# Performance work log

Measured on AMD Instinct MI355X. Metric: run time of the kernel, lower is better.

The kernel has to match this reference:

```python
import jax, jax.numpy as jnp
import numpy as np

I_SZ, H_SZ, M_SZ, D_SZ, T_LEN = 256, 512, 16384, 256, 128


def setup_inputs() -> dict:
    key = jax.random.key(0)
    ks = iter(jax.random.split(key, 48))

    def rn(shape, s=0.05):
        return jax.random.normal(next(ks), shape, dtype=jnp.float32) * s

    Hd, D = H_SZ, D_SZ
    inp = {
        "inputs": rn((T_LEN, 1, I_SZ), 1.0),
        "memory0": rn((M_SZ, D), 0.01),            # register_buffer: randn*0.01
        "read_w0": jnp.zeros((M_SZ,), jnp.float32),
        "write_w0": jnp.zeros((M_SZ,), jnp.float32),
        "W_ih": rn((4 * Hd, I_SZ + D)),             # LSTM input->gates (i,f,g,o)
        "W_hh": rn((4 * Hd, Hd)),
        "b_ih": jnp.zeros((4 * Hd,), jnp.float32),
        "b_hh": jnp.zeros((4 * Hd,), jnp.float32),
        "Wo": rn((I_SZ, Hd + D)),                   # output_layer
        "bo": jnp.zeros((I_SZ,), jnp.float32),
    }
    for p in ("r", "w"):  # read head / write head addressing params
        inp[p + "_Wk"] = rn((D, Hd)); inp[p + "_bk"] = jnp.zeros((D,), jnp.float32)
        inp[p + "_Wb"] = rn((1, Hd)); inp[p + "_bb"] = jnp.zeros((1,), jnp.float32)
        inp[p + "_Wg"] = rn((1, Hd)); inp[p + "_bg"] = jnp.zeros((1,), jnp.float32)
        inp[p + "_Ws"] = rn((3, Hd)); inp[p + "_bs"] = jnp.zeros((3,), jnp.float32)
        inp[p + "_Wp"] = rn((1, Hd)); inp[p + "_bp"] = jnp.zeros((1,), jnp.float32)
    inp["w_We"] = rn((D, Hd)); inp["w_be"] = jnp.zeros((D,), jnp.float32)  # erase
    inp["w_Wa"] = rn((D, Hd)); inp["w_ba"] = jnp.zeros((D,), jnp.float32)  # add
    return inp


def _attend(co, mem, prev_w, Wk, bk, Wb, bb, Wg, bg, Ws, bs, Wp, bp):
    # co: (1,H), mem: (M,D), prev_w: (M,) -> (M,)
    key = co @ Wk.T + bk                                   # (1,D)
    beta = jax.nn.softplus(co @ Wb.T + bb)                 # (1,1) key strength
    kn = key / jnp.maximum(jnp.linalg.norm(key, axis=-1, keepdims=True), 1e-12)
    mn = mem / jnp.maximum(jnp.linalg.norm(mem, axis=-1, keepdims=True), 1e-12)
    cw = jax.nn.softmax(beta * (kn @ mn.T), axis=-1)       # (1,M) content weights
    g = jax.nn.sigmoid(co @ Wg.T + bg)                     # interpolation gate
    gw = g * cw + (1.0 - g) * prev_w[None, :]
    s = jax.nn.softmax(co @ Ws.T + bs, axis=-1)            # (1,3) shift kernel
    shifted = (s[:, 0:1] * jnp.roll(gw, -1, axis=-1)
               + s[:, 1:2] * gw
               + s[:, 2:3] * jnp.roll(gw, 1, axis=-1))
    gamma = jax.nn.softplus(co @ Wp.T + bp) + 1.0          # sharpening >= 1
    w = shifted ** gamma
    return (w / (w.sum(-1, keepdims=True) + 1e-8))[0]


def reference(inputs, memory0, read_w0, write_w0, W_ih, W_hh, b_ih, b_hh, Wo, bo,
              r_Wk, r_bk, r_Wb, r_bb, r_Wg, r_bg, r_Ws, r_bs, r_Wp, r_bp,
              w_Wk, w_bk, w_Wb, w_bb, w_Wg, w_bg, w_Ws, w_bs, w_Wp, w_bp,
              w_We, w_be, w_Wa, w_ba):
    H = W_hh.shape[1]

    def step(carry, x_t):
        mem, rw, ww, h, c = carry
        read_vec = rw @ mem                                  # (D,) read old memory
        ci = jnp.concatenate([x_t[0], read_vec])[None, :]    # (1, I+D)
        gates = ci @ W_ih.T + b_ih + h @ W_hh.T + b_hh       # (1, 4H)
        i_, f_, g_, o_ = jnp.split(gates, 4, axis=-1)
        c_new = jax.nn.sigmoid(f_) * c + jax.nn.sigmoid(i_) * jnp.tanh(g_)
        h_new = jax.nn.sigmoid(o_) * jnp.tanh(c_new)
        co = h_new                                           # controller output (1,H)
        ww_new = _attend(co, mem, ww, w_Wk, w_bk, w_Wb, w_bb, w_Wg, w_bg, w_Ws, w_bs, w_Wp, w_bp)
        erase = jax.nn.sigmoid(co @ w_We.T + w_be)[0]        # (D,)
        add = (co @ w_Wa.T + w_ba)[0]                        # (D,)
        mem_new = mem * (1.0 - ww_new[:, None] * erase[None, :]) + ww_new[:, None] * add[None, :]
        rw_new = _attend(co, mem_new, rw, r_Wk, r_bk, r_Wb, r_bb, r_Wg, r_bg, r_Ws, r_bs, r_Wp, r_bp)
        out = jnp.concatenate([co[0], read_vec])[None, :] @ Wo.T + bo  # (1, I)
        return (mem_new, rw_new, ww_new, h_new, c_new), out

    init = (memory0, read_w0, write_w0,
            jnp.zeros((1, H), inputs.dtype), jnp.zeros((1, H), inputs.dtype))
    _, outs = jax.lax.scan(step, init, inputs)               # (T,1,I)
    return outs
```

## Files before the change

kernel.cpp:

```cpp
#include <hip/hip_runtime.h>
#include <math.h>


#define NBLK 128
#define NTHR 512
#define Msz  16384
#define Dsz  256
#define Hsz  512
#define Isz  256
#define Tlen 128
#define RPB  128
#define NG   16
#define PUBSTR 8

struct Params { const float* in[34]; float* out; float* ws; };

__device__ __forceinline__ float wred64(float v){
#pragma unroll
  for (int o = 32; o > 0; o >>= 1) v += __shfl_xor(v, o, 64);
  return v;
}
__device__ __forceinline__ float wred32(float v){
#pragma unroll
  for (int o = 16; o > 0; o >>= 1) v += __shfl_xor(v, o, 32);
  return v;
}
__device__ __forceinline__ float qsum4(float v){
  v += __uint_as_float(__builtin_amdgcn_mov_dpp(__float_as_uint(v), 0xB1, 0xF, 0xF, true));
  v += __uint_as_float(__builtin_amdgcn_mov_dpp(__float_as_uint(v), 0x4E, 0xF, 0xF, true));
  return v;
}
__device__ __forceinline__ float sigm(float x){ return 1.f / (1.f + __expf(-x)); }
__device__ __forceinline__ float softplusf(float x){ return (x > 20.f) ? x : log1pf(__expf(x)); }

__device__ __forceinline__ void gstore(float* p, float v){
  __hip_atomic_store(p, v, __ATOMIC_RELAXED, __HIP_MEMORY_SCOPE_AGENT);
}
__device__ __forceinline__ float gload(const float* p){
  return __hip_atomic_load(p, __ATOMIC_RELAXED, __HIP_MEMORY_SCOPE_AGENT);
}
__device__ __forceinline__ void gstore64(unsigned long long* p, unsigned long long v){
  __hip_atomic_store(p, v, __ATOMIC_RELAXED, __HIP_MEMORY_SCOPE_AGENT);
}
__device__ __forceinline__ unsigned long long gload64(const unsigned long long* p){
  return __hip_atomic_load(p, __ATOMIC_RELAXED, __HIP_MEMORY_SCOPE_AGENT);
}
__device__ __forceinline__ void lbar(){
  __builtin_amdgcn_s_waitcnt(0xC07F);
  __builtin_amdgcn_s_barrier();
}
__device__ __forceinline__ float pollw(const unsigned long long* p, unsigned want){
  unsigned long long k;
  do { k = gload64(p); } while ((int)((unsigned)(k >> 32) - want) < 0);
  return __uint_as_float((unsigned)k);
}

__global__ void __launch_bounds__(NTHR, 1)
ntm_kernel(Params P)
{
  const int b   = blockIdx.x;
  const int tid = threadIdx.x;
  const int wv  = tid >> 6;
  const int ln  = tid & 63;

  const float* inputs  = P.in[0];
  const float* mem0    = P.in[1];
  const float* read_w0 = P.in[2];
  const float* write_w0= P.in[3];
  const float* W_ih = P.in[4];
  const float* W_hh = P.in[5];
  const float* b_ih = P.in[6];
  const float* b_hh = P.in[7];
  const float* Wo   = P.in[8];
  const float* bo   = P.in[9];
  const float* r_Wk = P.in[10]; const float* r_bk = P.in[11];
  const float* r_Wb = P.in[12]; const float* r_bb = P.in[13];
  const float* r_Wg = P.in[14]; const float* r_bg = P.in[15];
  const float* r_Ws = P.in[16]; const float* r_bs = P.in[17];
  const float* r_Wp = P.in[18]; const float* r_bp = P.in[19];
  const float* w_Wk = P.in[20]; const float* w_bk = P.in[21];
  const float* w_Wb = P.in[22]; const float* w_bb = P.in[23];
  const float* w_Wg = P.in[24]; const float* w_bg = P.in[25];
  const float* w_Ws = P.in[26]; const float* w_bs = P.in[27];
  const float* w_Wp = P.in[28]; const float* w_bp = P.in[29];
  const float* w_We = P.in[30]; const float* w_be = P.in[31];
  const float* w_Wa = P.in[32]; const float* w_ba = P.in[33];
  float* out = P.out;

  float* ws = P.ws;
  float* PA = ws;
  float* PB = ws + 4096;
  unsigned long long* U    = (unsigned long long*)(ws + 8192);
  unsigned long long* hpub = U;
  unsigned long long* ppub = U + 1024;
  unsigned long long* pubD = U + 2320;
  unsigned long long* pubF = pubD + 1024;
  unsigned long long* pubH = pubF + 1024;
  unsigned long long* pubJ = pubH + 1024;
  unsigned long long* wEF = pubJ + 1024;
  unsigned long long* wPF = wEF + 128;
  unsigned long long* wEL = wPF + 128;
  unsigned long long* wPL = wEL + 128;
  unsigned long long* rEF = wPL + 128;
  unsigned long long* rPF = rEF + 128;
  unsigned long long* rEL = rPF + 128;
  unsigned long long* rPL = rEL + 128;
  float* Pbuf[2] = { PA, PB };

  __shared__ float s_mem[RPB * Dsz];
  __shared__ float s_co[Hsz];
  __shared__ float s_a[256], s_b[256], s_c[256];
  __shared__ float s_rv[256];
  __shared__ float s_norm[RPB];
  __shared__ float s_e[RPB];
  __shared__ float s_bw[RPB];
  __shared__ float s_rw[RPB];
  __shared__ float s_ww[RPB];
  __shared__ float s_A1[RPB], s_A2[RPB], s_B1[RPB], s_B0[RPB];
  __shared__ float s_dot[RPB];
  __shared__ float s_red[8];
  __shared__ float s_lg[16];
  __shared__ float s_scal[16];
  __shared__ float s_w2[2];
  __shared__ float s_cst[4];
  __shared__ float s_bd[4];
  __shared__ float s_pub;
  __shared__ float s_gval;

  auto pubWaitSum = [&](unsigned long long* pub, unsigned want)->float{
    if (wv == 0){
      const unsigned long long* p0 = &pub[(size_t)ln * PUBSTR];
      const unsigned long long* p1 = &pub[(size_t)(64 + ln) * PUBSTR];
      unsigned long long k0, k1;
      for (;;){
        k0 = gload64(p0); k1 = gload64(p1);
        bool ok = ((int)((unsigned)(k0 >> 32) - want) >= 0) &&
                  ((int)((unsigned)(k1 >> 32) - want) >= 0);
        if (__all(ok)) break;
      }
      float acc = __uint_as_float((unsigned)k0) + __uint_as_float((unsigned)k1);
      acc = wred64(acc);
      if (ln == 0) s_gval = acc;
    }
    lbar();
    return s_gval;
  };

  auto bred512 = [&](float v)->float{
    v = wred64(v);
    lbar();
    if (ln == 0) s_red[wv] = v;
    lbar();
    return s_red[0] + s_red[1] + s_red[2] + s_red[3]
         + s_red[4] + s_red[5] + s_red[6] + s_red[7];
  };

  auto shiftSharpen = [&](int si, float* s_prevw, float S,
                          unsigned long long* pub, unsigned tag){
    float g     = sigm(s_scal[si + 1]);
    float gamma = softplusf(s_scal[si + 2]) + 1.f;
    float a0 = s_scal[si + 3], a1 = s_scal[si + 4], a2 = s_scal[si + 5];
    float mx = fmaxf(a0, fmaxf(a1, a2));
    float e0 = __expf(a0 - mx), e1 = __expf(a1 - mx), e2 = __expf(a2 - mx);
    float idn = 1.f / (e0 + e1 + e2);
    float s0 = e0 * idn, s1 = e1 * idn, s2 = e2 * idn;
    float invS = 1.f / S;
    float w = 0.f;
    if (tid < RPB){
      float gc = g * invS, gp = 1.f - g;
      float em = s_e[tid],  pm = s_prevw[tid];
      float e1n = (tid < RPB-1) ? s_e[tid+1]     : s_bd[0];
      float p1n = (tid < RPB-1) ? s_prevw[tid+1] : s_bd[1];
      float e2n = (tid > 0)     ? s_e[tid-1]     : s_bd[2];
      float p2n = (tid > 0)     ? s_prevw[tid-1] : s_bd[3];
      float gwm = gc * em  + gp * pm;
      float gw1 = gc * e1n + gp * p1n;
      float gw2 = gc * e2n + gp * p2n;
      float sh = s0 * gw1 + s1 * gwm + s2 * gw2;
      w = powf(sh, gamma);
      s_bw[tid] = w;
    }
    float tot = wred64(w);
    if (ln == 0 && wv < 2) s_w2[wv] = tot;
    lbar();
    if (tid == 0){
      float T2 = s_w2[0] + s_w2[1];
      s_pub = T2;
      if (pub) gstore64(&pub[(size_t)b * PUBSTR],
                        ((unsigned long long)tag << 32) | (unsigned long long)__float_as_uint(T2));
    }
  };

  auto gemvXH = [&]()->float{
    int dd = tid >> 5, l = tid & 31;
    int r = (dd >> 2) * Hsz + (b << 2) + (dd & 3);
    const float* wi = W_ih + (size_t)r * (Isz + Dsz);
    const float* wh = W_hh + (size_t)r * Hsz;
    float acc = 0.f;
#pragma unroll
    for (int it = 0; it < 2; ++it){
      int k = it * 128 + l * 4;
      float4 a = *(const float4*)(wi + k);
      float4 x = *(const float4*)(&s_a[k]);
      acc += a.x*x.x + a.y*x.y + a.z*x.z + a.w*x.w;
    }
#pragma unroll
    for (int it = 0; it < 4; ++it){
      int k = it * 128 + l * 4;
      float4 hw = *(const float4*)(wh + k);
      float4 hv = *(const float4*)(&s_co[k]);
      acc += hw.x*hv.x + hw.y*hv.y + hw.z*hv.z + hw.w*hv.w;
    }
    return acc;
  };

  float Srcarry = 1.f;
  float accxh   = 0.f;

  {
    if (b < NG && tid < 256){ gstore(&PA[b*256 + tid], 0.f); gstore(&PB[b*256 + tid], 0.f); }
    if (tid < RPB){
      s_rw[tid] = read_w0[b * RPB + tid];
      s_ww[tid] = write_w0[b * RPB + tid];
    }
    if (tid < 4) s_cst[tid] = 0.f;
    s_co[tid] = 0.f;
    __syncthreads();
    if (tid == 0) gstore64(&pubD[(size_t)b * PUBSTR], (1ull << 32));
    pubWaitSum(pubD, 1);
  }

  {
#pragma unroll 1
    for (int it = 0; it < 16; ++it){
      int ml = it * 8 + wv;
      int m  = b * RPB + ml;
      float4 v = *(const float4*)(mem0 + (size_t)m * Dsz + ln * 4);
      *(float4*)(&s_mem[ml * Dsz + ln * 4]) = v;
      float n2 = wred64(v.x*v.x + v.y*v.y + v.z*v.z + v.w*v.w);
      if (ln == 0) s_norm[ml] = sqrtf(n2);
    }
    lbar();
    int col = tid & 255, half = tid >> 8;
    float acc = 0.f;
#pragma unroll 1
    for (int j = half * 64; j < half * 64 + 64; ++j) acc += s_rw[j] * s_mem[j * Dsz + col];
    if (half == 0) s_a[col] = acc;
    lbar();
    if (half == 1) atomicAdd(&PB[(b & (NG-1)) * 256 + col], acc + s_a[col]);
    __syncthreads();
    if (tid < 256) s_a[tid] = inputs[tid];
    if (tid == 0) gstore64(&pubD[(size_t)b * PUBSTR], (2ull << 32));
    lbar();
    accxh = gemvXH();
    pubWaitSum(pubD, 2);
  }

  for (int t = 0; t < Tlen; ++t){
    const unsigned TT = (unsigned)(t + 3);
    const unsigned long long tg = (unsigned long long)TT << 32;
    float* Pcur = Pbuf[t & 1];
    float* Prd  = Pbuf[(t + 1) & 1];

    {
      float SrDiv = (t == 0) ? 1.f : (Srcarry + 1e-8f);
      if (t > 0 && tid < RPB) s_rw[tid] = s_bw[tid] / SrDiv;
      if (tid < 256){
        float rvv = 0.f;
#pragma unroll
        for (int p = 0; p < NG; ++p) rvv += gload(&Prd[p * 256 + tid]);
        s_rv[tid] = rvv / SrDiv;
      }
      lbar();
      int dd = tid >> 5, l = tid & 31;
      int r = (dd >> 2) * Hsz + (b << 2) + (dd & 3);
      const float* wi = W_ih + (size_t)r * (Isz + Dsz) + Isz;
      float acc = accxh;
#pragma unroll
      for (int it = 0; it < 2; ++it){
        int k = it * 128 + l * 4;
        float4 a = *(const float4*)(wi + k);
        float4 x = *(const float4*)(&s_rv[k]);
        acc += a.x*x.x + a.y*x.y + a.z*x.z + a.w*x.w;
      }
      acc = wred32(acc);
      if (l == 0) s_lg[dd] = acc + b_ih[r] + b_hh[r];
      lbar();
      if (tid < 4){
        float iv = s_lg[tid], fv = s_lg[4 + tid], gv = s_lg[8 + tid], ov = s_lg[12 + tid];
        float cn = sigm(fv) * s_cst[tid] + sigm(iv) * tanhf(gv);
        s_cst[tid] = cn;
        float hn = sigm(ov) * tanhf(cn);
        gstore64(&hpub[(size_t)b * 8 + tid], tg | (unsigned long long)__float_as_uint(hn));
      }
    }

    {
      s_co[tid] = pollw(&hpub[(size_t)(tid >> 2) * 8 + (tid & 3)], TT);
      lbar();
#pragma unroll
      for (int qi = 0; qi < 2; ++qi){
        int q = qi * 8 + wv;
        int slot = q * 128 + b;
        if (slot < 1292){
          const float* Wrow = nullptr; float bias = 0.f; int len = 512;
          int mode = 0;
          if (slot < 256){ Wrow = w_Wk + (size_t)slot * Hsz; bias = w_bk[slot]; }
          else if (slot < 512){ int i = slot - 256; Wrow = w_We + (size_t)i * Hsz; bias = w_be[i]; mode = 1; }
          else if (slot < 768){ int i = slot - 512; Wrow = w_Wa + (size_t)i * Hsz; bias = w_ba[i]; }
          else if (slot < 1024){ int i = slot - 768; Wrow = r_Wk + (size_t)i * Hsz; bias = r_bk[i]; }
          else if (slot < 1280){ int i = slot - 1024; Wrow = Wo + (size_t)i * (Hsz + Dsz); bias = bo[i]; len = 768; mode = 2; }
          else {
            int i = slot - 1280;
            int ii = (i >= 6) ? i - 6 : i;
            bool rh = (i >= 6);
            const float *Wt, *bt; int row = 0;
            if (ii == 0){ Wt = rh ? r_Wb : w_Wb; bt = rh ? r_bb : w_bb; }
            else if (ii == 1){ Wt = rh ? r_Wg : w_Wg; bt = rh ? r_bg : w_bg; }
            else if (ii == 2){ Wt = rh ? r_Wp : w_Wp; bt = rh ? r_bp : w_bp; }
            else { Wt = rh ? r_Ws : w_Ws; bt = rh ? r_bs : w_bs; row = ii - 3; }
            Wrow = Wt + (size_t)row * Hsz; bias = bt[row];
          }
          float acc = 0.f;
          if (len == 512){
            int k = ln * 8;
            float4 a0 = *(const float4*)(Wrow + k);
            float4 a1 = *(const float4*)(Wrow + k + 4);
            float4 c0 = *(const float4*)(&s_co[k]);
            float4 c1 = *(const float4*)(&s_co[k + 4]);
            acc = a0.x*c0.x + a0.y*c0.y + a0.z*c0.z + a0.w*c0.w
                + a1.x*c1.x + a1.y*c1.y + a1.z*c1.z + a1.w*c1.w;
          } else {
#pragma unroll 1
            for (int kk = ln; kk < 768; kk += 64){
              float xv = (kk < Hsz) ? s_co[kk] : s_rv[kk - Hsz];
              acc += Wrow[kk] * xv;
            }
          }
          acc = wred64(acc);
          if (ln == 0){
            float v = acc + bias;
            if (mode == 1) v = sigm(v);
            if (mode == 2) out[(size_t)t * Isz + (slot - 1024)] = v;
            else gstore64(&ppub[slot], tg | (unsigned long long)__float_as_uint(v));
          }
        }
      }
    }

    if (t == Tlen - 1) break;

    float betaR = 0.f, invbkR = 0.f;

    {
      float* Pnx = Pbuf[(t + 1) & 1];
      if (b < NG && tid < 256) gstore(&Pnx[b * 256 + tid], 0.f);
      if (tid < 256) s_a[tid] = pollw(&ppub[tid], TT);
      else if (tid < 268) s_scal[tid - 256] = pollw(&ppub[1280 + (tid - 256)], TT);
      lbar();
      float nk2 = bred512((tid < 256) ? s_a[tid] * s_a[tid] : 0.f);
      float beta  = softplusf(s_scal[0]);
      float invbk = beta / fmaxf(sqrtf(nk2), 1e-12f);
      int row = tid >> 2, q = tid & 3;
      const float* mrow = &s_mem[row * Dsz];
      float d = 0.f;
#pragma unroll
      for (int k = 0; k < 16; ++k){
        int c = (q + 4 * ((k + row) & 15)) * 4;
        float4 mv = *(const float4*)(mrow + c);
        float4 kv = *(const float4*)(&s_a[c]);
        d += mv.x*kv.x + mv.y*kv.y + mv.z*kv.z + mv.w*kv.w;
      }
      d = qsum4(d);
      if (q == 0) s_dot[row] = d;
      lbar();
      float e = 0.f;
      if (tid < RPB){
        float score = s_dot[tid] * invbk / fmaxf(s_norm[tid], 1e-12f);
        e = __expf(score - beta);
        s_e[tid] = e;
      }
      float tot = wred64(e);
      if (ln == 0 && wv < 2) s_w2[wv] = tot;
      lbar();
      if (tid == 0){
        float T = s_w2[0] + s_w2[1];
        gstore64(&wEF[b], tg | (unsigned long long)__float_as_uint(s_e[0]));
        gstore64(&wPF[b], tg | (unsigned long long)__float_as_uint(s_ww[0]));
        gstore64(&wEL[b], tg | (unsigned long long)__float_as_uint(s_e[RPB-1]));
        gstore64(&wPL[b], tg | (unsigned long long)__float_as_uint(s_ww[RPB-1]));
        gstore64(&pubD[(size_t)b * PUBSTR], tg | (unsigned long long)__float_as_uint(T));
      }
    }

    {
      if (tid < 256) s_a[tid] = pollw(&ppub[256 + tid], TT);
      else           s_b[tid - 256] = pollw(&ppub[512 + (tid - 256)], TT);
      if (tid < 256) s_c[tid] = pollw(&ppub[768 + tid], TT);
      float nk2r = bred512((tid < 256) ? s_c[tid] * s_c[tid] : 0.f);
      betaR  = softplusf(s_scal[6]);
      invbkR = betaR / fmaxf(sqrtf(nk2r), 1e-12f);
      int row = tid >> 2, q = tid & 3;
      const float* mrow = &s_mem[row * Dsz];
      float mq = 0.f, qq = 0.f, qk = 0.f, mk = 0.f;
#pragma unroll
      for (int k = 0; k < 16; ++k){
        int c = (q + 4 * ((k + row) & 15)) * 4;
        float4 mv = *(const float4*)(mrow + c);
        float4 er = *(const float4*)(&s_a[c]);
        float4 ad = *(const float4*)(&s_b[c]);
        float4 kr = *(const float4*)(&s_c[c]);
        float qx = ad.x - mv.x * er.x;
        float qy = ad.y - mv.y * er.y;
        float qz = ad.z - mv.z * er.z;
        float qw = ad.w - mv.w * er.w;
        mq += mv.x*qx + mv.y*qy + mv.z*qz + mv.w*qw;
        qq += qx*qx + qy*qy + qz*qz + qw*qw;
        qk += qx*kr.x + qy*kr.y + qz*kr.z + qw*kr.w;
        mk += mv.x*kr.x + mv.y*kr.y + mv.z*kr.z + mv.w*kr.w;
      }
      mq = qsum4(mq); qq = qsum4(qq); qk = qsum4(qk); mk = qsum4(mk);
      if (q == 0){ s_A1[row] = 2.f*mq; s_A2[row] = qq; s_B1[row] = qk; s_B0[row] = mk; }
    }

    {
      if (wv == 0 && ln < 4){
        const unsigned long long* bp = (ln == 0) ? &wEF[(b + 1) & (NBLK-1)]
                               : (ln == 1) ? &wPF[(b + 1) & (NBLK-1)]
                               : (ln == 2) ? &wEL[(b - 1) & (NBLK-1)]
                                           : &wPL[(b - 1) & (NBLK-1)];
        s_bd[ln] = pollw(bp, TT);
      }
      float S_w = pubWaitSum(pubD, TT);
      shiftSharpen(0, s_ww, S_w, pubF, TT);
    }

    {
      float Sw = pubWaitSum(pubF, TT);
      float invSw = 1.f / (Sw + 1e-8f);
      float4 er4 = *(const float4*)(&s_a[ln * 4]);
      float4 ad4 = *(const float4*)(&s_b[ln * 4]);
#pragma unroll 1
      for (int it = 0; it < 16; ++it){
        int ml = it * 8 + wv;
        int off = ml * Dsz + ln * 4;
        float wwm = s_bw[ml] * invSw;
        float4 mv = *(const float4*)(&s_mem[off]);
        float4 nv;
        nv.x = fmaf(wwm, ad4.x - mv.x * er4.x, mv.x);
        nv.y = fmaf(wwm, ad4.y - mv.y * er4.y, mv.y);
        nv.z = fmaf(wwm, ad4.z - mv.z * er4.z, mv.z);
        nv.w = fmaf(wwm, ad4.w - mv.w * er4.w, mv.w);
        *(float4*)(&s_mem[off]) = nv;
      }
      float e = 0.f;
      if (tid < RPB){
        float wwm = s_bw[tid] * invSw;
        s_ww[tid] = wwm;
        float A0 = s_norm[tid] * s_norm[tid];
        float n2 = fmaf(wwm, fmaf(wwm, s_A2[tid], s_A1[tid]), A0);
        float dt = fmaf(wwm, s_B1[tid], s_B0[tid]);
        float nr = sqrtf(fmaxf(n2, 0.f));
        s_norm[tid] = nr;
        float score = dt * invbkR / fmaxf(nr, 1e-12f);
        e = __expf(score - betaR);
        s_e[tid] = e;
      }
      float tot = wred64(e);
      if (ln == 0 && wv < 2) s_w2[wv] = tot;
      lbar();
      if (tid == 0){
        float T2 = s_w2[0] + s_w2[1];
        gstore64(&rEF[b], tg | (unsigned long long)__float_as_uint(s_e[0]));
        gstore64(&rPF[b], tg | (unsigned long long)__float_as_uint(s_rw[0]));
        gstore64(&rEL[b], tg | (unsigned long long)__float_as_uint(s_e[RPB-1]));
        gstore64(&rPL[b], tg | (unsigned long long)__float_as_uint(s_rw[RPB-1]));
        gstore64(&pubH[(size_t)b * PUBSTR], tg | (unsigned long long)__float_as_uint(T2));
      }
    }

    {
      if (wv == 0 && ln < 4){
        const unsigned long long* bp = (ln == 0) ? &rEF[(b + 1) & (NBLK-1)]
                               : (ln == 1) ? &rPF[(b + 1) & (NBLK-1)]
                               : (ln == 2) ? &rEL[(b - 1) & (NBLK-1)]
                                           : &rPL[(b - 1) & (NBLK-1)];
        s_bd[ln] = pollw(bp, TT);
      }
      float S_r = pubWaitSum(pubH, TT);
      shiftSharpen(6, s_rw, S_r, nullptr, 0);
      lbar();
      int col = tid & 255, half = tid >> 8;
      float acc = 0.f;
#pragma unroll 1
      for (int j = half * 64; j < half * 64 + 64; ++j) acc += s_bw[j] * s_mem[j * Dsz + col];
      if (half == 0) s_a[col] = acc;
      lbar();
      if (half == 1) atomicAdd(&Pcur[(b & (NG-1)) * 256 + col], acc + s_a[col]);
      __syncthreads();
      if (tid == 0)
        gstore64(&pubJ[(size_t)b * PUBSTR], tg | (unsigned long long)__float_as_uint(s_pub));
      if (tid < 256) s_a[tid] = inputs[(size_t)(t + 1) * Isz + tid];
      lbar();
      accxh = gemvXH();
      Srcarry = pubWaitSum(pubJ, TT);
    }
  }
}

extern "C" void kernel_launch(void* const* d_in, const int* in_sizes, int n_in,
                              void* d_out, int out_size, void* d_ws, size_t ws_size,
                              hipStream_t stream)
{
  (void)in_sizes; (void)out_size;
  if (n_in < 34) return;
  if (ws_size < (size_t)98304) return;
  Params P;
  for (int i = 0; i < 34; ++i) P.in[i] = (const float*)d_in[i];
  P.out = (float*)d_out;
  P.ws  = (float*)d_ws;
  hipLaunchKernelGGL(ntm_kernel, dim3(NBLK), dim3(NTHR), 0, stream, P);
}
```

Before: 3.664 ms.

## Replace per-block publish-and-gather sums with fixed-point atomic grid reductions

Grid-wide partial sums were previously gathered by having each block publish a tagged value and then polling all 128 slots with a wavefront. They are now accumulated into one 64-bit slot per timestep and stage: the high bits count arrivals and the low bits hold a fixed-point sum, so one thread polls a single address. The read-head content scores are also computed and published before the memory write loop rather than after it, so neighbouring blocks can proceed sooner. The output GEMV inner loop is vectorised with float4 loads. Fixed-point truncation slightly changes numerics, and correctness relies on the counter slots starting at zero.

```diff
diff --git a/kernel.cpp b/kernel.cpp
--- a/kernel.cpp
+++ b/kernel.cpp
@@ -11,7 +11,10 @@
 #define Tlen 128
 #define RPB  128
 #define NG   16
-#define PUBSTR 8
+
+#define FXS  1073741824.0f
+#define FXSI (1.0 / 1073741824.0)
+#define CNT1 (1ull << 48)
 
 struct Params { const float* in[34]; float* out; float* ws; };
 
@@ -53,6 +56,9 @@
   unsigned long long k;
   do { k = gload64(p); } while ((int)((unsigned)(k >> 32) - want) < 0);
   return __uint_as_float((unsigned)k);
+}
+__device__ __forceinline__ unsigned long long fxpack(float v){
+  return CNT1 + (unsigned long long)(v * FXS);
 }
 
 __global__ void __launch_bounds__(NTHR, 1)
@@ -93,18 +99,19 @@
   unsigned long long* U    = (unsigned long long*)(ws + 8192);
   unsigned long long* hpub = U;
   unsigned long long* ppub = U + 1024;
-  unsigned long long* pubD = U + 2320;
-  unsigned long long* pubF = pubD + 1024;
-  unsigned long long* pubH = pubF + 1024;
-  unsigned long long* pubJ = pubH + 1024;
-  unsigned long long* wEF = pubJ + 1024;
-  unsigned long long* wPF = wEF + 128;
-  unsigned long long* wEL = wPF + 128;
-  unsigned long long* wPL = wEL + 128;
-  unsigned long long* rEF = wPL + 128;
-  unsigned long long* rPF = rEF + 128;
-  unsigned long long* rEL = rPF + 128;
-  unsigned long long* rPL = rEL + 128;
+  unsigned long long* wEF  = U + 2320;
+  unsigned long long* wPF  = wEF + 128;
+  unsigned long long* wEL  = wPF + 128;
+  unsigned long long* wPL  = wEL + 128;
+  unsigned long long* rEF  = wPL + 128;
+  unsigned long long* rPF  = rEF + 128;
+  unsigned long long* rEL  = rPF + 128;
+  unsigned long long* rPL  = rEL + 128;
+  unsigned long long* redD = rPL + 128;
+  unsigned long long* redF = redD + Tlen;
+  unsigned long long* redH = redF + Tlen;
+  unsigned long long* redJ = redH + Tlen;
+  unsigned long long* redI = redJ + Tlen;
   float* Pbuf[2] = { PA, PB };
 
   __shared__ float s_mem[RPB * Dsz];
@@ -127,20 +134,11 @@
   __shared__ float s_pub;
   __shared__ float s_gval;
 
-  auto pubWaitSum = [&](unsigned long long* pub, unsigned want)->float{
-    if (wv == 0){
-      const unsigned long long* p0 = &pub[(size_t)ln * PUBSTR];
-      const unsigned long long* p1 = &pub[(size_t)(64 + ln) * PUBSTR];
-      unsigned long long k0, k1;
-      for (;;){
-        k0 = gload64(p0); k1 = gload64(p1);
-        bool ok = ((int)((unsigned)(k0 >> 32) - want) >= 0) &&
-                  ((int)((unsigned)(k1 >> 32) - want) >= 0);
-        if (__all(ok)) break;
-      }
-      float acc = __uint_as_float((unsigned)k0) + __uint_as_float((unsigned)k1);
-      acc = wred64(acc);
-      if (ln == 0) s_gval = acc;
+  auto redWait = [&](unsigned long long* slot)->float{
+    if (tid == 0){
+      unsigned long long k;
+      do { k = gload64(slot); } while ((unsigned)(k >> 48) < (unsigned)NBLK);
+      s_gval = (float)((double)(k & 0xFFFFFFFFFFFFull) * FXSI);
     }
     lbar();
     return s_gval;
@@ -155,8 +153,7 @@
          + s_red[4] + s_red[5] + s_red[6] + s_red[7];
   };
 
-  auto shiftSharpen = [&](int si, float* s_prevw, float S,
-                          unsigned long long* pub, unsigned tag){
+  auto shiftSharpen = [&](int si, float* s_prevw, float S, unsigned long long* slot){
     float g     = sigm(s_scal[si + 1]);
     float gamma = softplusf(s_scal[si + 2]) + 1.f;
     float a0 = s_scal[si + 3], a1 = s_scal[si + 4], a2 = s_scal[si + 5];
@@ -186,8 +183,7 @@
     if (tid == 0){
       float T2 = s_w2[0] + s_w2[1];
       s_pub = T2;
-      if (pub) gstore64(&pub[(size_t)b * PUBSTR],
-                        ((unsigned long long)tag << 32) | (unsigned long long)__float_as_uint(T2));
+      if (slot) atomicAdd(slot, fxpack(T2));
     }
   };
 
@@ -226,8 +222,8 @@
     if (tid < 4) s_cst[tid] = 0.f;
     s_co[tid] = 0.f;
     __syncthreads();
-    if (tid == 0) gstore64(&pubD[(size_t)b * PUBSTR], (1ull << 32));
-    pubWaitSum(pubD, 1);
+    if (tid == 0) atomicAdd(redI + 0, CNT1);
+    redWait(redI + 0);
   }
 
   {
@@ -250,10 +246,10 @@
     if (half == 1) atomicAdd(&PB[(b & (NG-1)) * 256 + col], acc + s_a[col]);
     __syncthreads();
     if (tid < 256) s_a[tid] = inputs[tid];
-    if (tid == 0) gstore64(&pubD[(size_t)b * PUBSTR], (2ull << 32));
+    if (tid == 0) atomicAdd(redI + 1, CNT1);
     lbar();
     accxh = gemvXH();
-    pubWaitSum(pubD, 2);
+    redWait(redI + 1);
   }
 
   for (int t = 0; t < Tlen; ++t){
@@ -331,11 +327,16 @@
             acc = a0.x*c0.x + a0.y*c0.y + a0.z*c0.z + a0.w*c0.w
                 + a1.x*c1.x + a1.y*c1.y + a1.z*c1.z + a1.w*c1.w;
           } else {
-#pragma unroll 1
-            for (int kk = ln; kk < 768; kk += 64){
-              float xv = (kk < Hsz) ? s_co[kk] : s_rv[kk - Hsz];
-              acc += Wrow[kk] * xv;
-            }
+            int k = ln * 4;
+            float4 w0 = *(const float4*)(Wrow + k);
+            float4 w1 = *(const float4*)(Wrow + 256 + k);
+            float4 w2 = *(const float4*)(Wrow + 512 + k);
+            float4 c0 = *(const float4*)(&s_co[k]);
+            float4 c1 = *(const float4*)(&s_co[256 + k]);
+            float4 r0 = *(const float4*)(&s_rv[k]);
+            acc = w0.x*c0.x + w0.y*c0.y + w0.z*c0.z + w0.w*c0.w
+                + w1.x*c1.x + w1.y*c1.y + w1.z*c1.z + w1.w*c1.w
+                + w2.x*r0.x + w2.y*r0.y + w2.z*r0.z + w2.w*r0.w;
           }
           acc = wred64(acc);
           if (ln == 0){
@@ -389,7 +390,7 @@
         gstore64(&wPF[b], tg | (unsigned long long)__float_as_uint(s_ww[0]));
         gstore64(&wEL[b], tg | (unsigned long long)__float_as_uint(s_e[RPB-1]));
         gstore64(&wPL[b], tg | (unsigned long long)__float_as_uint(s_ww[RPB-1]));
-        gstore64(&pubD[(size_t)b * PUBSTR], tg | (unsigned long long)__float_as_uint(T));
+        atomicAdd(redD + t, fxpack(T));
       }
     }
 
@@ -431,15 +432,39 @@
                                            : &wPL[(b - 1) & (NBLK-1)];
         s_bd[ln] = pollw(bp, TT);
       }
-      float S_w = pubWaitSum(pubD, TT);
-      shiftSharpen(0, s_ww, S_w, pubF, TT);
-    }
-
-    {
-      float Sw = pubWaitSum(pubF, TT);
+      float S_w = redWait(redD + t);
+      shiftSharpen(0, s_ww, S_w, redF + t);
+    }
+
+    {
+      float Sw = redWait(redF + t);
       float invSw = 1.f / (Sw + 1e-8f);
       float4 er4 = *(const float4*)(&s_a[ln * 4]);
       float4 ad4 = *(const float4*)(&s_b[ln * 4]);
+      float e = 0.f;
+      if (tid < RPB){
+        float wwm = s_bw[tid] * invSw;
+        s_ww[tid] = wwm;
+        float A0 = s_norm[tid] * s_norm[tid];
+        float n2 = fmaf(wwm, fmaf(wwm, s_A2[tid], s_A1[tid]), A0);
+        float dt = fmaf(wwm, s_B1[tid], s_B0[tid]);
+        float nr = sqrtf(fmaxf(n2, 0.f));
+        s_norm[tid] = nr;
+        float score = dt * invbkR / fmaxf(nr, 1e-12f);
+        e = __expf(score - betaR);
+        s_e[tid] = e;
+      }
+      float tot = wred64(e);
+      if (ln == 0 && wv < 2) s_w2[wv] = tot;
+      lbar();
+      if (tid == 0){
+        float T2 = s_w2[0] + s_w2[1];
+        gstore64(&rEF[b], tg | (unsigned long long)__float_as_uint(s_e[0]));
+        gstore64(&rPF[b], tg | (unsigned long long)__float_as_uint(s_rw[0]));
+        gstore64(&rEL[b], tg | (unsigned long long)__float_as_uint(s_e[RPB-1]));
+        gstore64(&rPL[b], tg | (unsigned long long)__float_as_uint(s_rw[RPB-1]));
+        atomicAdd(redH + t, fxpack(T2));
+      }
 #pragma unroll 1
       for (int it = 0; it < 16; ++it){
         int ml = it * 8 + wv;
@@ -453,30 +478,6 @@
         nv.w = fmaf(wwm, ad4.w - mv.w * er4.w, mv.w);
         *(float4*)(&s_mem[off]) = nv;
       }
-      float e = 0.f;
-      if (tid < RPB){
-        float wwm = s_bw[tid] * invSw;
-        s_ww[tid] = wwm;
-        float A0 = s_norm[tid] * s_norm[tid];
-        float n2 = fmaf(wwm, fmaf(wwm, s_A2[tid], s_A1[tid]), A0);
-        float dt = fmaf(wwm, s_B1[tid], s_B0[tid]);
-        float nr = sqrtf(fmaxf(n2, 0.f));
-        s_norm[tid] = nr;
-        float score = dt * invbkR / fmaxf(nr, 1e-12f);
-        e = __expf(score - betaR);
-        s_e[tid] = e;
-      }
-      float tot = wred64(e);
-      if (ln == 0 && wv < 2) s_w2[wv] = tot;
-      lbar();
-      if (tid == 0){
-        float T2 = s_w2[0] + s_w2[1];
-        gstore64(&rEF[b], tg | (unsigned long long)__float_as_uint(s_e[0]));
-        gstore64(&rPF[b], tg | (unsigned long long)__float_as_uint(s_rw[0]));
-        gstore64(&rEL[b], tg | (unsigned long long)__float_as_uint(s_e[RPB-1]));
-        gstore64(&rPL[b], tg | (unsigned long long)__float_as_uint(s_rw[RPB-1]));
-        gstore64(&pubH[(size_t)b * PUBSTR], tg | (unsigned long long)__float_as_uint(T2));
-      }
     }
 
     {
@@ -487,8 +488,8 @@
                                            : &rPL[(b - 1) & (NBLK-1)];
         s_bd[ln] = pollw(bp, TT);
       }
-      float S_r = pubWaitSum(pubH, TT);
-      shiftSharpen(6, s_rw, S_r, nullptr, 0);
+      float S_r = redWait(redH + t);
+      shiftSharpen(6, s_rw, S_r, nullptr);
       lbar();
       int col = tid & 255, half = tid >> 8;
       float acc = 0.f;
@@ -498,12 +499,11 @@
       lbar();
       if (half == 1) atomicAdd(&Pcur[(b & (NG-1)) * 256 + col], acc + s_a[col]);
       __syncthreads();
-      if (tid == 0)
-        gstore64(&pubJ[(size_t)b * PUBSTR], tg | (unsigned long long)__float_as_uint(s_pub));
+      if (tid == 0) atomicAdd(redJ + t, fxpack(s_pub));
       if (tid < 256) s_a[tid] = inputs[(size_t)(t + 1) * Isz + tid];
       lbar();
       accxh = gemvXH();
-      Srcarry = pubWaitSum(pubJ, TT);
+      Srcarry = redWait(redJ + t);
     }
   }
 }
```

Measured after the change: 3.631 ms. Within noise of the previous version (-0.9%).
